# Performance work log

Measured on AMD Instinct MI355X. Metric: run time of the kernel, lower is better.

The kernel has to match this reference:

```python
import jax, jax.numpy as jnp
import numpy as np

# Config mirrors module init: C=12 channels, include_time=True -> d=13, depth=3
# sig_channels = d + d^2 + d^3 = 2379

def setup_inputs() -> dict:
    key = jax.random.key(0)
    k1, k2, k3 = jax.random.split(key, 3)
    N, C, J, T, L = 8, 12, 25, 64, 5
    d = C + 1
    sig_channels = d + d * d + d ** 3  # 2379
    out_dim = 256
    x = jax.random.normal(k1, (N, C, J, T, L), dtype=jnp.float32)
    W = jax.random.normal(k2, (out_dim, sig_channels), dtype=jnp.float32) / np.sqrt(sig_channels)
    b = jax.random.normal(k3, (out_dim,), dtype=jnp.float32) * 0.01
    return {"x": x, "W": W, "b": b}


def _signature_depth3(path):
    """Truncated (depth 3) path signature with zero basepoint.
    path: [B, L, d] -> sig: [B, d + d^2 + d^3]
    Chen's identity: s <- s * exp(dx), with exp(dx)_n = dx^{(x)n} / n!
    """
    B, L, d = path.shape
    # basepoint=True: prepend zeros, then take increments
    inc = jnp.diff(jnp.concatenate([jnp.zeros((B, 1, d), path.dtype), path], axis=1), axis=1)  # [B, L, d]

    def step(carry, dx):
        s1, s2, s3 = carry  # [B,d], [B,d*d], [B,d^3]
        e2 = 0.5 * jnp.einsum('bi,bj->bij', dx, dx)                     # [B,d,d]
        e3 = (jnp.einsum('bij,bk->bijk', e2, dx) / 3.0).reshape(B, d ** 3)  # dx^3/6
        n1 = s1 + dx
        n2 = s2 + jnp.einsum('bi,bj->bij', s1, dx).reshape(B, d * d) + e2.reshape(B, d * d)
        n3 = (s3
              + jnp.einsum('bij,bk->bijk', s2.reshape(B, d, d), dx).reshape(B, d ** 3)
              + jnp.einsum('bi,bjk->bijk', s1, e2).reshape(B, d ** 3)
              + e3)
        return (n1, n2, n3), None

    init = (jnp.zeros((B, d), path.dtype),
            jnp.zeros((B, d * d), path.dtype),
            jnp.zeros((B, d ** 3), path.dtype))
    (s1, s2, s3), _ = jax.lax.scan(step, init, jnp.moveaxis(inc, 1, 0))
    return jnp.concatenate([s1, s2, s3], axis=-1)


def reference(x, W, b):
    N, C, J, T, L = x.shape
    B = J * T * N
    # windowed gather: block (i*T+j)*N..(..+1)*N = x[:,:,i,j,:].permute(0,2,1)
    path = jnp.transpose(x, (2, 3, 0, 4, 1)).reshape(B, L, C)  # [J*T*N, L, C]
    # Augment include_time=True: append time channel linspace(0,1,L)
    t = jnp.linspace(0.0, 1.0, L, dtype=path.dtype)
    path = jnp.concatenate([path, jnp.broadcast_to(t[None, :, None], (B, L, 1))], axis=-1)
    sig = _signature_depth3(path)                 # [B, 2379]
    z = sig @ W.T + b                             # [B, out_dim]
    # scatter back: res[:, :, i, j] = z[(i*T+j)*N : ...]
    return jnp.transpose(z.reshape(J, T, N, -1), (2, 3, 0, 1))  # [N, out_dim, J, T]
```

## Files before the change

### kernel.cpp

```cpp
#include <hip/hip_runtime.h>
#include <hip/hip_bf16.h>

typedef float f32x4 __attribute__((ext_vector_type(4)));
typedef short s16x8 __attribute__((ext_vector_type(8)));

#define SIGC 2379
#define KPAD 2432
#define NKT  76
#define NKT_HALF 38
#define SROW 2440
#define NPATH 12800


__device__ inline void split2(float v, __hip_bfloat16* h, __hip_bfloat16* l) {
    __hip_bfloat16 hh = __float2bfloat16(v);
    *h = hh;
    *l = __float2bfloat16(v - __bfloat162float(hh));
}

__device__ inline void gload_lds16(const __hip_bfloat16* g, __hip_bfloat16* l) {
    __builtin_amdgcn_global_load_lds(
        (const __attribute__((address_space(1))) void*)g,
        (__attribute__((address_space(3))) void*)l,
        16, 0, 0);
}

__global__ __launch_bounds__(256) void wconv_kernel(const float* __restrict__ W,
                                                    __hip_bfloat16* __restrict__ Wh,
                                                    __hip_bfloat16* __restrict__ Wl)
{
    int k = blockIdx.x * 256 + threadIdx.x;
    int n = blockIdx.y;
    if (k >= KPAD) return;
    float v = (k < SIGC) ? W[(size_t)n * SIGC + k] : 0.0f;
    size_t off = ((size_t)(n >> 4) * NKT + (k >> 5)) * 512 + ((k >> 3) & 3) * 128 + (n & 15) * 8 + (k & 7);
    split2(v, &Wh[off], &Wl[off]);
}

__global__ __launch_bounds__(256) void sig_kernel(const float* __restrict__ x,
                                                  __hip_bfloat16* __restrict__ Ah,
                                                  __hip_bfloat16* __restrict__ Al_,
                                                  int r_start)
{
    __shared__ float inc_s[4][5][16];
    __shared__ __align__(16) __hip_bfloat16 hi_s[4][SROW];
    __shared__ __align__(16) __hip_bfloat16 lo_s[4][SROW];

    const int t = threadIdx.x;
    const int w = t >> 6;
    const int lane = t & 63;

    const int p0 = lane;
    const int p1 = lane + 64;
    const int p2 = lane + 128;
    const bool has2 = (p2 < 169);
    const int i0 = p0 / 13, j0 = p0 - i0 * 13;
    const int i1 = p1 / 13, j1 = p1 - i1 * 13;
    const int i2 = p2 / 13, j2 = p2 - i2 * 13;

    for (int pp = 0; pp < 4; ++pp) {
        const int r = r_start + blockIdx.x * 16 + pp * 4 + w;
        const int nn = r & 7;
        const int jj = (r >> 3) & 63;
        const int ii = r >> 9;

        __syncthreads();
        if (lane < 13) {
            if (lane < 12) {
                const float* px = x + ((size_t)(nn * 12 + lane) * 1600 + ii * 64 + jj) * 5;
                float prev = 0.0f;
                #pragma unroll
                for (int l = 0; l < 5; ++l) {
                    float v = px[l];
                    inc_s[w][l][lane] = v - prev;
                    prev = v;
                }
            } else {
                inc_s[w][0][12] = 0.0f;
                #pragma unroll
                for (int l = 1; l < 5; ++l) inc_s[w][l][12] = 0.25f;
            }
        }
        __syncthreads();

        float s1i0 = 0.0f, s1i1 = 0.0f, s1i2 = 0.0f;
        float s2p0 = 0.0f, s2p1 = 0.0f, s2p2 = 0.0f;
        float s1own = 0.0f;
        float s3a[13], s3b[13], s3c[13];
        #pragma unroll
        for (int k = 0; k < 13; ++k) { s3a[k] = 0.0f; s3b[k] = 0.0f; s3c[k] = 0.0f; }

        for (int l = 0; l < 5; ++l) {
            float dxl[13];
            #pragma unroll
            for (int k = 0; k < 13; ++k) dxl[k] = inc_s[w][l][k];

            {
                float dxi = inc_s[w][l][i0];
                float dxj = inc_s[w][l][j0];
                float C   = s2p0 + 0.5f * dxj * (s1i0 + dxi * (1.0f / 3.0f));
                #pragma unroll
                for (int k = 0; k < 13; ++k) s3a[k] += dxl[k] * C;
                s2p0 += s1i0 * dxj + 0.5f * dxi * dxj;
                s1i0 += dxi;
            }
            {
                float dxi = inc_s[w][l][i1];
                float dxj = inc_s[w][l][j1];
                float C   = s2p1 + 0.5f * dxj * (s1i1 + dxi * (1.0f / 3.0f));
                #pragma unroll
                for (int k = 0; k < 13; ++k) s3b[k] += dxl[k] * C;
                s2p1 += s1i1 * dxj + 0.5f * dxi * dxj;
                s1i1 += dxi;
            }
            if (has2) {
                float dxi = inc_s[w][l][i2];
                float dxj = inc_s[w][l][j2];
                float C   = s2p2 + 0.5f * dxj * (s1i2 + dxi * (1.0f / 3.0f));
                #pragma unroll
                for (int k = 0; k < 13; ++k) s3c[k] += dxl[k] * C;
                s2p2 += s1i2 * dxj + 0.5f * dxi * dxj;
                s1i2 += dxi;
            }
            if (lane < 13) s1own += inc_s[w][l][lane];
        }

        if (lane < 13) split2(s1own, &hi_s[w][lane], &lo_s[w][lane]);
        split2(s2p0, &hi_s[w][13 + p0], &lo_s[w][13 + p0]);
        split2(s2p1, &hi_s[w][13 + p1], &lo_s[w][13 + p1]);
        if (has2) split2(s2p2, &hi_s[w][13 + p2], &lo_s[w][13 + p2]);
        #pragma unroll
        for (int k = 0; k < 13; ++k) split2(s3a[k], &hi_s[w][182 + p0 * 13 + k], &lo_s[w][182 + p0 * 13 + k]);
        #pragma unroll
        for (int k = 0; k < 13; ++k) split2(s3b[k], &hi_s[w][182 + p1 * 13 + k], &lo_s[w][182 + p1 * 13 + k]);
        if (has2) {
            #pragma unroll
            for (int k = 0; k < 13; ++k) split2(s3c[k], &hi_s[w][182 + p2 * 13 + k], &lo_s[w][182 + p2 * 13 + k]);
        }
        if (lane < KPAD - SIGC) {
            hi_s[w][SIGC + lane] = __float2bfloat16(0.0f);
            lo_s[w][SIGC + lane] = __float2bfloat16(0.0f);
        }

        __syncthreads();

        const int rtl = blockIdx.x;
        const int rr = t & 3, ks = (t >> 2) & 3, ts = t >> 4;
        #pragma unroll
        for (int it2 = 0; it2 < 5; ++it2) {
            int kt = it2 * 16 + ts;
            if (kt < NKT) {
                size_t off = ((size_t)rtl * NKT + kt) * 512 + ks * 128 + (pp * 4 + rr) * 8;
                int lidx = kt * 32 + ks * 8;
                *reinterpret_cast<int4*>(Ah + off)  = *reinterpret_cast<const int4*>(&hi_s[rr][lidx]);
                *reinterpret_cast<int4*>(Al_ + off) = *reinterpret_cast<const int4*>(&lo_s[rr][lidx]);
            }
        }
    }
}

__global__ __launch_bounds__(256) void gemm_kernel(const __hip_bfloat16* __restrict__ Ah,
                                                   const __hip_bfloat16* __restrict__ Al_,
                                                   const __hip_bfloat16* __restrict__ Wh,
                                                   const __hip_bfloat16* __restrict__ Wl,
                                                   float* __restrict__ P,
                                                   int chunk_alloc, int nmblk)
{
    __shared__ __align__(16) __hip_bfloat16 L[2][24 * 512];

    const int bid = blockIdx.x;
    const int x8 = bid & 7;
    const int h = (bid >> 3) & 1;
    const int ksp = (bid >> 4) & 1;
    const int q = bid >> 5;
    const int mIdx = q * 8 + x8;
    if (mIdx >= nmblk) return;

    const int t = threadIdx.x;
    const int lane = t & 63;
    const int w = t >> 6;
    const int wm = w >> 1, wn = w & 1;
    const int rt0 = mIdx * 4;
    const int nt0 = h * 8;
    const int kt0 = ksp * NKT_HALF;

    f32x4 acc[2][4] = {};

    auto stage = [&](int buf, int kt) {
        #pragma unroll
        for (int s = 0; s < 6; ++s) {
            int tt = w * 6 + s;
            const __hip_bfloat16* g;
            if (tt < 4)       g = Ah  + ((size_t)(rt0 + tt)      * NKT + kt) * 512;
            else if (tt < 8)  g = Al_ + ((size_t)(rt0 + tt - 4)  * NKT + kt) * 512;
            else if (tt < 16) g = Wh  + ((size_t)(nt0 + tt - 8)  * NKT + kt) * 512;
            else              g = Wl  + ((size_t)(nt0 + tt - 16) * NKT + kt) * 512;
            gload_lds16(g + lane * 8, &L[buf][tt * 512]);
        }
    };

    stage(0, kt0);
    int cur = 0;
    __syncthreads();

    for (int kk = 0; kk < NKT_HALF; ++kk) {
        if (kk + 1 < NKT_HALF) stage(cur ^ 1, kt0 + kk + 1);

        const int fb = (lane >> 4) * 128 + (lane & 15) * 8;
        s16x8 ah[2], al4[2], bh[4], bl4[4];
        #pragma unroll
        for (int mm = 0; mm < 2; ++mm) {
            int base = (2 * wm + mm) * 512 + fb;
            ah[mm]  = *reinterpret_cast<const s16x8*>(&L[cur][base]);
            al4[mm] = *reinterpret_cast<const s16x8*>(&L[cur][2048 + base]);
        }
        #pragma unroll
        for (int nn = 0; nn < 4; ++nn) {
            int base = (4 * wn + nn) * 512 + fb;
            bh[nn]  = *reinterpret_cast<const s16x8*>(&L[cur][4096 + base]);
            bl4[nn] = *reinterpret_cast<const s16x8*>(&L[cur][8192 + base]);
        }

        #pragma unroll
        for (int mm = 0; mm < 2; ++mm)
            #pragma unroll
            for (int nn = 0; nn < 4; ++nn) {
                acc[mm][nn] = __builtin_amdgcn_mfma_f32_16x16x32_bf16(ah[mm],  bh[nn],  acc[mm][nn], 0, 0, 0);
                acc[mm][nn] = __builtin_amdgcn_mfma_f32_16x16x32_bf16(ah[mm],  bl4[nn], acc[mm][nn], 0, 0, 0);
                acc[mm][nn] = __builtin_amdgcn_mfma_f32_16x16x32_bf16(al4[mm], bh[nn],  acc[mm][nn], 0, 0, 0);
            }

        __syncthreads();
        cur ^= 1;
    }

    float* Pb = P + ((size_t)ksp * chunk_alloc + mIdx * 64) * 256 + h * 128;
    #pragma unroll
    for (int mm = 0; mm < 2; ++mm)
        #pragma unroll
        for (int nn = 0; nn < 4; ++nn) {
            int o = wn * 64 + nn * 16 + (lane & 15);
            #pragma unroll
            for (int rr = 0; rr < 4; ++rr) {
                int p = wm * 32 + mm * 16 + (lane >> 4) * 4 + rr;
                Pb[(size_t)p * 256 + o] = acc[mm][nn][rr];
            }
        }
}

__global__ __launch_bounds__(256) void reduce_kernel(const float* __restrict__ P,
                                                     const float* __restrict__ b,
                                                     float* __restrict__ out,
                                                     int chunk_alloc, int r_start)
{
    const int mb = blockIdx.x;
    const int pbase = r_start + mb * 64;
    const int ii = pbase >> 9;
    const int jj0 = (pbase >> 3) & 63;
    const int t = threadIdx.x;
    const int ol = t >> 1, hh = t & 1;

    const float* P0 = P + (size_t)mb * 64 * 256;
    const float* P1 = P0 + (size_t)chunk_alloc * 256;

    #pragma unroll
    for (int oh = 0; oh < 2; ++oh) {
        int o = oh * 128 + ol;
        float bo = b[o];
        #pragma unroll
        for (int c = 0; c < 4; ++c) {
            int ni = hh * 4 + c;
            float v[8];
            #pragma unroll
            for (int qq = 0; qq < 8; ++qq) {
                size_t idx = (size_t)(qq * 8 + ni) * 256 + o;
                v[qq] = P0[idx] + P1[idx] + bo;
            }
            float* dst = out + (size_t)(ni * 256 + o) * 1600 + ii * 64 + jj0;
            *reinterpret_cast<float4*>(dst)     = make_float4(v[0], v[1], v[2], v[3]);
            *reinterpret_cast<float4*>(dst + 4) = make_float4(v[4], v[5], v[6], v[7]);
        }
    }
}

extern "C" void kernel_launch(void* const* d_in, const int* in_sizes, int n_in,
                              void* d_out, int out_size, void* d_ws, size_t ws_size,
                              hipStream_t stream)
{
    const float* x = (const float*)d_in[0];
    const float* W = (const float*)d_in[1];
    const float* b = (const float*)d_in[2];
    float* out = (float*)d_out;

    char* ws = (char*)d_ws;
    __hip_bfloat16* Wh = (__hip_bfloat16*)ws;
    __hip_bfloat16* Wl = Wh + (size_t)16 * NKT * 512;
    size_t a_off = (((size_t)16 * NKT * 512 * 2 * 2) + 255) & ~(size_t)255;

    size_t avail = (ws_size > a_off) ? ws_size - a_off : 0;
    long long maxp = (long long)(avail / ((size_t)KPAD * 4 + 2048));
    int chunk = (int)((maxp / 64) * 64);
    if (chunk > NPATH) chunk = NPATH;
    if (chunk < 64) chunk = 64;

    __hip_bfloat16* Ah = (__hip_bfloat16*)(ws + a_off);
    __hip_bfloat16* Al_ = Ah + (size_t)chunk * KPAD;
    float* P = (float*)(Al_ + (size_t)chunk * KPAD);

    wconv_kernel<<<dim3(10, 256), 256, 0, stream>>>(W, Wh, Wl);

    for (int r0 = 0; r0 < NPATH; r0 += chunk) {
        int cnt = NPATH - r0;
        if (cnt > chunk) cnt = chunk;
        int nmblk = cnt / 64;
        int nblk = ((nmblk + 7) / 8) * 32;
        sig_kernel<<<dim3(cnt / 16), 256, 0, stream>>>(x, Ah, Al_, r0);
        gemm_kernel<<<dim3(nblk), 256, 0, stream>>>(Ah, Al_, Wh, Wl, P, chunk, nmblk);
        reduce_kernel<<<dim3(cnt / 64), 256, 0, stream>>>(P, b, out, chunk, r0);
    }
}
```

Before: 124.8 us.

## Restructure GEMM to full-N tiles with 4-way split-K and direct W loads

The GEMM now has each block compute a 64-row tile over all 256 output columns, with the K dimension split four ways instead of two. Only the A hi/lo tiles are staged in LDS; each wave reads its W fragments straight from global memory (expected to hit L2), which shrinks LDS use and removes the W staging traffic. The reduce kernel now sums four partial buffers and is launched on a 2D grid split over output halves. The cost is more partial-sum traffic through global memory and W fragment loads issued inside the MFMA loop without LDS double buffering, which may stall the wave.

```diff
diff --git a/kernel.cpp b/kernel.cpp
--- a/kernel.cpp
+++ b/kernel.cpp
@@ -7,7 +7,7 @@
 #define SIGC 2379
 #define KPAD 2432
 #define NKT  76
-#define NKT_HALF 38
+#define NKT_Q 19
 #define SROW 2440
 #define NPATH 12800
 
@@ -166,83 +166,70 @@
                                                    float* __restrict__ P,
                                                    int chunk_alloc, int nmblk)
 {
-    __shared__ __align__(16) __hip_bfloat16 L[2][24 * 512];
+    __shared__ __align__(16) __hip_bfloat16 L[2][8 * 512];
 
     const int bid = blockIdx.x;
     const int x8 = bid & 7;
-    const int h = (bid >> 3) & 1;
-    const int ksp = (bid >> 4) & 1;
-    const int q = bid >> 5;
-    const int mIdx = q * 8 + x8;
+    const int ksp = x8 >> 1;
+    const int bb = x8 & 1;
+    const int k2 = bid >> 3;
+    const int mIdx = k2 * 2 + bb;
     if (mIdx >= nmblk) return;
 
     const int t = threadIdx.x;
     const int lane = t & 63;
     const int w = t >> 6;
-    const int wm = w >> 1, wn = w & 1;
     const int rt0 = mIdx * 4;
-    const int nt0 = h * 8;
-    const int kt0 = ksp * NKT_HALF;
-
-    f32x4 acc[2][4] = {};
+    const int kt0 = ksp * NKT_Q;
+
+    f32x4 acc[4][4] = {};
 
     auto stage = [&](int buf, int kt) {
-        #pragma unroll
-        for (int s = 0; s < 6; ++s) {
-            int tt = w * 6 + s;
-            const __hip_bfloat16* g;
-            if (tt < 4)       g = Ah  + ((size_t)(rt0 + tt)      * NKT + kt) * 512;
-            else if (tt < 8)  g = Al_ + ((size_t)(rt0 + tt - 4)  * NKT + kt) * 512;
-            else if (tt < 16) g = Wh  + ((size_t)(nt0 + tt - 8)  * NKT + kt) * 512;
-            else              g = Wl  + ((size_t)(nt0 + tt - 16) * NKT + kt) * 512;
-            gload_lds16(g + lane * 8, &L[buf][tt * 512]);
-        }
+        gload_lds16(Ah  + ((size_t)(rt0 + w) * NKT + kt) * 512 + lane * 8, &L[buf][w * 512]);
+        gload_lds16(Al_ + ((size_t)(rt0 + w) * NKT + kt) * 512 + lane * 8, &L[buf][(4 + w) * 512]);
     };
 
     stage(0, kt0);
     int cur = 0;
     __syncthreads();
 
-    for (int kk = 0; kk < NKT_HALF; ++kk) {
-        if (kk + 1 < NKT_HALF) stage(cur ^ 1, kt0 + kk + 1);
-
-        const int fb = (lane >> 4) * 128 + (lane & 15) * 8;
-        s16x8 ah[2], al4[2], bh[4], bl4[4];
-        #pragma unroll
-        for (int mm = 0; mm < 2; ++mm) {
-            int base = (2 * wm + mm) * 512 + fb;
-            ah[mm]  = *reinterpret_cast<const s16x8*>(&L[cur][base]);
-            al4[mm] = *reinterpret_cast<const s16x8*>(&L[cur][2048 + base]);
-        }
+    for (int kk = 0; kk < NKT_Q; ++kk) {
+        const int kt = kt0 + kk;
+        if (kk + 1 < NKT_Q) stage(cur ^ 1, kt + 1);
+
+        s16x8 ah[4], al4[4];
+        #pragma unroll
+        for (int mm = 0; mm < 4; ++mm) {
+            ah[mm]  = *reinterpret_cast<const s16x8*>(&L[cur][mm * 512 + lane * 8]);
+            al4[mm] = *reinterpret_cast<const s16x8*>(&L[cur][(4 + mm) * 512 + lane * 8]);
+        }
+
         #pragma unroll
         for (int nn = 0; nn < 4; ++nn) {
-            int base = (4 * wn + nn) * 512 + fb;
-            bh[nn]  = *reinterpret_cast<const s16x8*>(&L[cur][4096 + base]);
-            bl4[nn] = *reinterpret_cast<const s16x8*>(&L[cur][8192 + base]);
-        }
-
-        #pragma unroll
-        for (int mm = 0; mm < 2; ++mm)
+            const size_t wo = ((size_t)(w * 4 + nn) * NKT + kt) * 512 + lane * 8;
+            s16x8 bh  = *reinterpret_cast<const s16x8*>(Wh + wo);
+            s16x8 bl4 = *reinterpret_cast<const s16x8*>(Wl + wo);
             #pragma unroll
-            for (int nn = 0; nn < 4; ++nn) {
-                acc[mm][nn] = __builtin_amdgcn_mfma_f32_16x16x32_bf16(ah[mm],  bh[nn],  acc[mm][nn], 0, 0, 0);
-                acc[mm][nn] = __builtin_amdgcn_mfma_f32_16x16x32_bf16(ah[mm],  bl4[nn], acc[mm][nn], 0, 0, 0);
-                acc[mm][nn] = __builtin_amdgcn_mfma_f32_16x16x32_bf16(al4[mm], bh[nn],  acc[mm][nn], 0, 0, 0);
-            }
+            for (int mm = 0; mm < 4; ++mm) {
+                acc[mm][nn] = __builtin_amdgcn_mfma_f32_16x16x32_bf16(ah[mm],  bh,  acc[mm][nn], 0, 0, 0);
+                acc[mm][nn] = __builtin_amdgcn_mfma_f32_16x16x32_bf16(ah[mm],  bl4, acc[mm][nn], 0, 0, 0);
+                acc[mm][nn] = __builtin_amdgcn_mfma_f32_16x16x32_bf16(al4[mm], bh,  acc[mm][nn], 0, 0, 0);
+            }
+        }
 
         __syncthreads();
         cur ^= 1;
     }
 
-    float* Pb = P + ((size_t)ksp * chunk_alloc + mIdx * 64) * 256 + h * 128;
+    float* Pb = P + ((size_t)ksp * chunk_alloc + mIdx * 64) * 256;
     #pragma unroll
-    for (int mm = 0; mm < 2; ++mm)
+    for (int mm = 0; mm < 4; ++mm)
         #pragma unroll
         for (int nn = 0; nn < 4; ++nn) {
-            int o = wn * 64 + nn * 16 + (lane & 15);
+            int o = w * 64 + nn * 16 + (lane & 15);
             #pragma unroll
             for (int rr = 0; rr < 4; ++rr) {
-                int p = wm * 32 + mm * 16 + (lane >> 4) * 4 + rr;
+                int p = mm * 16 + (lane >> 4) * 4 + rr;
                 Pb[(size_t)p * 256 + o] = acc[mm][nn][rr];
             }
         }
@@ -261,25 +248,22 @@
     const int ol = t >> 1, hh = t & 1;
 
     const float* P0 = P + (size_t)mb * 64 * 256;
-    const float* P1 = P0 + (size_t)chunk_alloc * 256;
-
+    const size_t ps = (size_t)chunk_alloc * 256;
+
+    int o = blockIdx.y * 128 + ol;
+    float bo = b[o];
     #pragma unroll
-    for (int oh = 0; oh < 2; ++oh) {
-        int o = oh * 128 + ol;
-        float bo = b[o];
-        #pragma unroll
-        for (int c = 0; c < 4; ++c) {
-            int ni = hh * 4 + c;
-            float v[8];
-            #pragma unroll
-            for (int qq = 0; qq < 8; ++qq) {
-                size_t idx = (size_t)(qq * 8 + ni) * 256 + o;
-                v[qq] = P0[idx] + P1[idx] + bo;
-            }
-            float* dst = out + (size_t)(ni * 256 + o) * 1600 + ii * 64 + jj0;
-            *reinterpret_cast<float4*>(dst)     = make_float4(v[0], v[1], v[2], v[3]);
-            *reinterpret_cast<float4*>(dst + 4) = make_float4(v[4], v[5], v[6], v[7]);
-        }
+    for (int c = 0; c < 4; ++c) {
+        int ni = hh * 4 + c;
+        float v[8];
+        #pragma unroll
+        for (int qq = 0; qq < 8; ++qq) {
+            size_t idx = (size_t)(qq * 8 + ni) * 256 + o;
+            v[qq] = P0[idx] + P0[idx + ps] + P0[idx + 2 * ps] + P0[idx + 3 * ps] + bo;
+        }
+        float* dst = out + (size_t)(ni * 256 + o) * 1600 + ii * 64 + jj0;
+        *reinterpret_cast<float4*>(dst)     = make_float4(v[0], v[1], v[2], v[3]);
+        *reinterpret_cast<float4*>(dst + 4) = make_float4(v[4], v[5], v[6], v[7]);
     }
 }
 
@@ -298,7 +282,7 @@
     size_t a_off = (((size_t)16 * NKT * 512 * 2 * 2) + 255) & ~(size_t)255;
 
     size_t avail = (ws_size > a_off) ? ws_size - a_off : 0;
-    long long maxp = (long long)(avail / ((size_t)KPAD * 4 + 2048));
+    long long maxp = (long long)(avail / ((size_t)KPAD * 4 + 4096));
     int chunk = (int)((maxp / 64) * 64);
     if (chunk > NPATH) chunk = NPATH;
     if (chunk < 64) chunk = 64;
@@ -313,9 +297,9 @@
         int cnt = NPATH - r0;
         if (cnt > chunk) cnt = chunk;
         int nmblk = cnt / 64;
-        int nblk = ((nmblk + 7) / 8) * 32;
+        int nblk = ((nmblk + 1) / 2) * 8;
         sig_kernel<<<dim3(cnt / 16), 256, 0, stream>>>(x, Ah, Al_, r0);
         gemm_kernel<<<dim3(nblk), 256, 0, stream>>>(Ah, Al_, Wh, Wl, P, chunk, nmblk);
-        reduce_kernel<<<dim3(cnt / 64), 256, 0, stream>>>(P, b, out, chunk, r0);
+        reduce_kernel<<<dim3(cnt / 64, 2), 256, 0, stream>>>(P, b, out, chunk, r0);
     }
 }
```

Result: slower. 135.1 us (+8.3%).

## Enlarge GEMM M-tile to 128 rows with triple-buffered LDS pipeline

Applied to the files above, without the earlier changes.

Each GEMM block now covers 128 path rows instead of 64, so every W tile staged into LDS is reused across twice as many rows. The double buffer becomes a three-stage LDS ring that uses explicit vmcnt waits and raw barriers, with MFMA sections raised in priority via setprio, to keep loads further ahead of compute. The reduce kernel is split across a second grid dimension over output halves. In exchange, LDS per block grows to 96KB and the grid shrinks to about 416 blocks, which may hurt occupancy and latency hiding on a 256-CU part.

```diff
diff --git a/kernel.cpp b/kernel.cpp
--- a/kernel.cpp
+++ b/kernel.cpp
@@ -166,7 +166,7 @@
                                                    float* __restrict__ P,
                                                    int chunk_alloc, int nmblk)
 {
-    __shared__ __align__(16) __hip_bfloat16 L[2][24 * 512];
+    __shared__ __align__(16) __hip_bfloat16 L[3][32 * 512];
 
     const int bid = blockIdx.x;
     const int x8 = bid & 7;
@@ -180,69 +180,75 @@
     const int lane = t & 63;
     const int w = t >> 6;
     const int wm = w >> 1, wn = w & 1;
-    const int rt0 = mIdx * 4;
+    const int rt0 = mIdx * 8;
     const int nt0 = h * 8;
     const int kt0 = ksp * NKT_HALF;
 
-    f32x4 acc[2][4] = {};
+    f32x4 acc[4][4] = {};
 
     auto stage = [&](int buf, int kt) {
         #pragma unroll
-        for (int s = 0; s < 6; ++s) {
-            int tt = w * 6 + s;
+        for (int s = 0; s < 8; ++s) {
+            int tt = w * 8 + s;
             const __hip_bfloat16* g;
-            if (tt < 4)       g = Ah  + ((size_t)(rt0 + tt)      * NKT + kt) * 512;
-            else if (tt < 8)  g = Al_ + ((size_t)(rt0 + tt - 4)  * NKT + kt) * 512;
-            else if (tt < 16) g = Wh  + ((size_t)(nt0 + tt - 8)  * NKT + kt) * 512;
-            else              g = Wl  + ((size_t)(nt0 + tt - 16) * NKT + kt) * 512;
+            if (tt < 8)       g = Ah  + ((size_t)(rt0 + tt)       * NKT + kt) * 512;
+            else if (tt < 16) g = Al_ + ((size_t)(rt0 + tt - 8)   * NKT + kt) * 512;
+            else if (tt < 24) g = Wh  + ((size_t)(nt0 + tt - 16)  * NKT + kt) * 512;
+            else              g = Wl  + ((size_t)(nt0 + tt - 24)  * NKT + kt) * 512;
             gload_lds16(g + lane * 8, &L[buf][tt * 512]);
         }
     };
 
-    stage(0, kt0);
-    int cur = 0;
-    __syncthreads();
-
-    for (int kk = 0; kk < NKT_HALF; ++kk) {
-        if (kk + 1 < NKT_HALF) stage(cur ^ 1, kt0 + kk + 1);
-
-        const int fb = (lane >> 4) * 128 + (lane & 15) * 8;
-        s16x8 ah[2], al4[2], bh[4], bl4[4];
-        #pragma unroll
-        for (int mm = 0; mm < 2; ++mm) {
-            int base = (2 * wm + mm) * 512 + fb;
-            ah[mm]  = *reinterpret_cast<const s16x8*>(&L[cur][base]);
-            al4[mm] = *reinterpret_cast<const s16x8*>(&L[cur][2048 + base]);
+    auto compute = [&](int lb) {
+        const __hip_bfloat16* Lb = &L[lb][0];
+        s16x8 ah[4], al4[4], bh[4], bl4[4];
+        #pragma unroll
+        for (int mm = 0; mm < 4; ++mm) {
+            ah[mm]  = *reinterpret_cast<const s16x8*>(&Lb[(wm * 4 + mm) * 512 + lane * 8]);
+            al4[mm] = *reinterpret_cast<const s16x8*>(&Lb[(8 + wm * 4 + mm) * 512 + lane * 8]);
         }
         #pragma unroll
         for (int nn = 0; nn < 4; ++nn) {
-            int base = (4 * wn + nn) * 512 + fb;
-            bh[nn]  = *reinterpret_cast<const s16x8*>(&L[cur][4096 + base]);
-            bl4[nn] = *reinterpret_cast<const s16x8*>(&L[cur][8192 + base]);
-        }
-
-        #pragma unroll
-        for (int mm = 0; mm < 2; ++mm)
+            bh[nn]  = *reinterpret_cast<const s16x8*>(&Lb[(16 + wn * 4 + nn) * 512 + lane * 8]);
+            bl4[nn] = *reinterpret_cast<const s16x8*>(&Lb[(24 + wn * 4 + nn) * 512 + lane * 8]);
+        }
+        __builtin_amdgcn_s_setprio(1);
+        #pragma unroll
+        for (int nn = 0; nn < 4; ++nn)
             #pragma unroll
-            for (int nn = 0; nn < 4; ++nn) {
+            for (int mm = 0; mm < 4; ++mm) {
                 acc[mm][nn] = __builtin_amdgcn_mfma_f32_16x16x32_bf16(ah[mm],  bh[nn],  acc[mm][nn], 0, 0, 0);
                 acc[mm][nn] = __builtin_amdgcn_mfma_f32_16x16x32_bf16(ah[mm],  bl4[nn], acc[mm][nn], 0, 0, 0);
                 acc[mm][nn] = __builtin_amdgcn_mfma_f32_16x16x32_bf16(al4[mm], bh[nn],  acc[mm][nn], 0, 0, 0);
             }
-
-        __syncthreads();
-        cur ^= 1;
+        __builtin_amdgcn_s_setprio(0);
+    };
+
+    stage(0, kt0);
+    stage(1, kt0 + 1);
+
+    #pragma unroll 1
+    for (int kk = 0; kk < NKT_HALF; ++kk) {
+        if (kk + 2 < NKT_HALF) stage((kk + 2) % 3, kt0 + kk + 2);
+        if (kk + 2 < NKT_HALF)      asm volatile("s_waitcnt vmcnt(16)" ::: "memory");
+        else if (kk + 1 < NKT_HALF) asm volatile("s_waitcnt vmcnt(8)" ::: "memory");
+        else                        asm volatile("s_waitcnt vmcnt(0)" ::: "memory");
+        __builtin_amdgcn_s_barrier();
+        asm volatile("" ::: "memory");
+        compute(kk % 3);
+        asm volatile("" ::: "memory");
+        __builtin_amdgcn_s_barrier();
     }
 
-    float* Pb = P + ((size_t)ksp * chunk_alloc + mIdx * 64) * 256 + h * 128;
+    float* Pb = P + ((size_t)ksp * chunk_alloc + mIdx * 128) * 256 + h * 128;
     #pragma unroll
-    for (int mm = 0; mm < 2; ++mm)
+    for (int mm = 0; mm < 4; ++mm)
         #pragma unroll
         for (int nn = 0; nn < 4; ++nn) {
             int o = wn * 64 + nn * 16 + (lane & 15);
             #pragma unroll
             for (int rr = 0; rr < 4; ++rr) {
-                int p = wm * 32 + mm * 16 + (lane >> 4) * 4 + rr;
+                int p = wm * 64 + mm * 16 + (lane >> 4) * 4 + rr;
                 Pb[(size_t)p * 256 + o] = acc[mm][nn][rr];
             }
         }
@@ -261,25 +267,22 @@
     const int ol = t >> 1, hh = t & 1;
 
     const float* P0 = P + (size_t)mb * 64 * 256;
-    const float* P1 = P0 + (size_t)chunk_alloc * 256;
-
+    const size_t ps = (size_t)chunk_alloc * 256;
+
+    int o = blockIdx.y * 128 + ol;
+    float bo = b[o];
     #pragma unroll
-    for (int oh = 0; oh < 2; ++oh) {
-        int o = oh * 128 + ol;
-        float bo = b[o];
-        #pragma unroll
-        for (int c = 0; c < 4; ++c) {
-            int ni = hh * 4 + c;
-            float v[8];
-            #pragma unroll
-            for (int qq = 0; qq < 8; ++qq) {
-                size_t idx = (size_t)(qq * 8 + ni) * 256 + o;
-                v[qq] = P0[idx] + P1[idx] + bo;
-            }
-            float* dst = out + (size_t)(ni * 256 + o) * 1600 + ii * 64 + jj0;
-            *reinterpret_cast<float4*>(dst)     = make_float4(v[0], v[1], v[2], v[3]);
-            *reinterpret_cast<float4*>(dst + 4) = make_float4(v[4], v[5], v[6], v[7]);
-        }
+    for (int c = 0; c < 4; ++c) {
+        int ni = hh * 4 + c;
+        float v[8];
+        #pragma unroll
+        for (int qq = 0; qq < 8; ++qq) {
+            size_t idx = (size_t)(qq * 8 + ni) * 256 + o;
+            v[qq] = P0[idx] + P0[idx + ps] + bo;
+        }
+        float* dst = out + (size_t)(ni * 256 + o) * 1600 + ii * 64 + jj0;
+        *reinterpret_cast<float4*>(dst)     = make_float4(v[0], v[1], v[2], v[3]);
+        *reinterpret_cast<float4*>(dst + 4) = make_float4(v[4], v[5], v[6], v[7]);
     }
 }
 
@@ -299,9 +302,9 @@
 
     size_t avail = (ws_size > a_off) ? ws_size - a_off : 0;
     long long maxp = (long long)(avail / ((size_t)KPAD * 4 + 2048));
-    int chunk = (int)((maxp / 64) * 64);
+    int chunk = (int)((maxp / 128) * 128);
     if (chunk > NPATH) chunk = NPATH;
-    if (chunk < 64) chunk = 64;
+    if (chunk < 128) chunk = 128;
 
     __hip_bfloat16* Ah = (__hip_bfloat16*)(ws + a_off);
     __hip_bfloat16* Al_ = Ah + (size_t)chunk * KPAD;
@@ -312,10 +315,10 @@
     for (int r0 = 0; r0 < NPATH; r0 += chunk) {
         int cnt = NPATH - r0;
         if (cnt > chunk) cnt = chunk;
-        int nmblk = cnt / 64;
+        int nmblk = cnt / 128;
         int nblk = ((nmblk + 7) / 8) * 32;
         sig_kernel<<<dim3(cnt / 16), 256, 0, stream>>>(x, Ah, Al_, r0);
         gemm_kernel<<<dim3(nblk), 256, 0, stream>>>(Ah, Al_, Wh, Wl, P, chunk, nmblk);
-        reduce_kernel<<<dim3(cnt / 64), 256, 0, stream>>>(P, b, out, chunk, r0);
+        reduce_kernel<<<dim3(cnt / 64, 2), 256, 0, stream>>>(P, b, out, chunk, r0);
     }
 }
```

After: 125.8 us. About the same (+0.8%).
